# Performance work log

Measured on AMD Instinct MI355X. Metric: run time of the kernel, lower is better.

Reference implementation:

```python
import jax, jax.numpy as jnp
import numpy as np

B, U, V = 2, 32, 2048
IN_DIM, STATE, CODE = 256, 512, 256
H, HD = 8, 64
INNER = H * HD  # 512
HID = STATE     # ffn capacity_factor = 1.0


def layernorm(x, g, b, eps=1e-5):
    mu = jnp.mean(x, axis=-1, keepdims=True)
    var = jnp.var(x, axis=-1, keepdims=True)
    return (x - mu) * jax.lax.rsqrt(var + eps) * g + b


def setup_inputs() -> dict:
    key = jax.random.key(0)
    ks = jax.random.split(key, 24)
    s = 0.02
    inp = {
        'receiver_states': jax.random.normal(ks[0], (B, U, STATE), jnp.float32),
        'receiver_signatures': jax.random.normal(ks[1], (B, U, 64), jnp.float32),
        'receiver_codes': jax.random.normal(ks[2], (B, U, CODE), jnp.float32),
        'sender_states': jax.random.normal(ks[3], (B, V, IN_DIM), jnp.float32),
        # layernorms
        'ln_s_g': jnp.ones((IN_DIM,), jnp.float32), 'ln_s_b': jnp.zeros((IN_DIM,), jnp.float32),
        'ln_r_g': jnp.ones((STATE,), jnp.float32), 'ln_r_b': jnp.zeros((STATE,), jnp.float32),
        # ModFC query: in=STATE out=INNER ctx=CODE
        'Wq': jax.random.normal(ks[4], (INNER, STATE), jnp.float32) * s,
        'bq': jnp.zeros((INNER,), jnp.float32),
        'Cq': jax.random.normal(ks[5], (STATE, CODE), jnp.float32) * s,
        # ModFC key/value: in=IN_DIM out=INNER ctx=CODE
        'Wk': jax.random.normal(ks[6], (INNER, IN_DIM), jnp.float32) * s,
        'bk': jnp.zeros((INNER,), jnp.float32),
        'Ck': jax.random.normal(ks[7], (IN_DIM, CODE), jnp.float32) * s,
        'Wv': jax.random.normal(ks[8], (INNER, IN_DIM), jnp.float32) * s,
        'bv': jnp.zeros((INNER,), jnp.float32),
        'Cv': jax.random.normal(ks[9], (IN_DIM, CODE), jnp.float32) * s,
        # exit ModFC: in=INNER out=STATE ctx=CODE
        'We': jax.random.normal(ks[10], (STATE, INNER), jnp.float32) * s,
        'be': jnp.zeros((STATE,), jnp.float32),
        'Ce': jax.random.normal(ks[11], (INNER, CODE), jnp.float32) * s,
        'ls_attn': jnp.ones((STATE,), jnp.float32) * 1.0,
        # FFN
        'ln_f_g': jnp.ones((STATE,), jnp.float32), 'ln_f_b': jnp.zeros((STATE,), jnp.float32),
        'W1': jax.random.normal(ks[12], (HID, STATE), jnp.float32) * s,
        'b1': jnp.zeros((HID,), jnp.float32),
        'C1': jax.random.normal(ks[13], (STATE, CODE), jnp.float32) * s,
        'W2': jax.random.normal(ks[14], (STATE, HID), jnp.float32) * s,
        'b2': jnp.zeros((STATE,), jnp.float32),
        'C2': jax.random.normal(ks[15], (HID, CODE), jnp.float32) * s,
        'ls_ffn': jnp.ones((STATE,), jnp.float32) * 1e-6,
    }
    return inp


def reference(receiver_states, receiver_signatures, receiver_codes, sender_states,
              ln_s_g, ln_s_b, ln_r_g, ln_r_b,
              Wq, bq, Cq, Wk, bk, Ck, Wv, bv, Cv, We, be, Ce, ls_attn,
              ln_f_g, ln_f_b, W1, b1, C1, W2, b2, C2, ls_ffn):
    codes = receiver_codes  # (b,u,code)
    # --- ReadInAttention ---
    r_ln = layernorm(receiver_states, ln_r_g, ln_r_b)           # (b,u,state)
    s_ln = layernorm(sender_states, ln_s_g, ln_s_b)             # (b,v,in)
    # ModFC: y = linear(x * (1 + code @ C))
    # queries: (b,u,inner)
    q = jnp.einsum('bus,is->bui', r_ln * (1.0 + jnp.einsum('buc,sc->bus', codes, Cq)), Wq) + bq
    # per-receiver modulated senders: scale (b,u,in) broadcast over v
    scale_k = 1.0 + jnp.einsum('buc,ic->bui', codes, Ck)        # (b,u,in)
    scale_v = 1.0 + jnp.einsum('buc,ic->bui', codes, Cv)        # (b,u,in)
    mod_k = s_ln[:, :, None, :] * scale_k[:, None, :, :]        # (b,v,u,in)
    mod_v = s_ln[:, :, None, :] * scale_v[:, None, :, :]        # (b,v,u,in)
    keys = jnp.einsum('bvui,oi->bvuo', mod_k, Wk) + bk          # (b,v,u,inner)
    values = jnp.einsum('bvui,oi->bvuo', mod_v, Wv) + bv        # (b,v,u,inner)
    keys = keys.reshape(B, V, U, H, HD).transpose(0, 3, 2, 1, 4)    # (b,h,u,v,c)
    values = values.reshape(B, V, U, H, HD).transpose(0, 3, 2, 1, 4)
    qh = q.reshape(B, U, H, HD).transpose(0, 2, 1, 3)           # (b,h,u,c)
    scores = jnp.einsum('bhuc,bhuvc->bhuv', qh, keys) / np.sqrt(HD)
    attn = jax.nn.softmax(scores, axis=-1)
    msg = jnp.einsum('bhuv,bhuvc->bhuc', attn, values)          # (b,h,u,c)
    msg = msg.transpose(0, 2, 1, 3).reshape(B, U, INNER)        # (b,u,inner)
    msg = jnp.einsum('bui,oi->buo', msg * (1.0 + jnp.einsum('buc,ic->bui', codes, Ce)), We) + be
    attn_out = msg * ls_attn  # include_residual=False in read-in attention
    # --- ModFFN (residual) ---
    x = attn_out
    r = layernorm(x, ln_f_g, ln_f_b)
    h1 = jnp.einsum('bus,os->buo', r * (1.0 + jnp.einsum('buc,sc->bus', codes, C1)), W1) + b1
    h1 = jax.nn.gelu(h1, approximate=False)
    h2 = jnp.einsum('buh,oh->buo', h1 * (1.0 + jnp.einsum('buc,hc->buh', codes, C2)), W2) + b2
    out = x + h2 * ls_ffn
    return out
```

## Files before the change

### kernel.cpp

```cpp
#include <hip/hip_runtime.h>
#include <math.h>

#define B_ 2
#define U_ 32
#define V_ 2048
#define IN_ 256
#define ST_ 512
#define H_ 8
#define BU_ 64
#define NR_ 512

#define WS_SLN   0u
#define WS_SLNT  1048576u
#define WS_SCALE 2097152u
#define WS_T     2260992u
#define WS_CB    2392064u
#define WS_SSUMP 2392576u
#define WS_CTXP  2396672u
#define WS_AO    3445248u
#define WS_H2    3478016u
#define WS_AOP   3510784u

__device__ __forceinline__ float wsum(float v){
  #pragma unroll
  for(int m=32;m>0;m>>=1) v += __shfl_xor(v, m, 64);
  return v;
}

#define FMA4(A, t, S) { A.x += (t)*(S).x; A.y += (t)*(S).y; A.z += (t)*(S).z; A.w += (t)*(S).w; }

__global__ __launch_bounds__(256) void k_pre(const float* __restrict__ snd,
    const float* __restrict__ g, const float* __restrict__ bb,
    const float* __restrict__ codes,
    const float* __restrict__ Cq, const float* __restrict__ Ck, const float* __restrict__ Cv,
    const float* __restrict__ Ce, const float* __restrict__ C1, const float* __restrict__ C2,
    float* __restrict__ ws){
  __shared__ float tile[32][261];
  __shared__ float cds[8][256];
  const int tid = threadIdx.x;
  if(blockIdx.x < 128){
    const int wave = tid>>6, lane = tid&63;
    const int rowbase = blockIdx.x * 32;
    const int b = rowbase >> 11, vloc = rowbase & 2047;
    float4 gg  = *(const float4*)(g  + lane*4);
    float4 bbv = *(const float4*)(bb + lane*4);
    for(int it=0; it<8; ++it){
      int rl = it*4 + wave;
      int r  = rowbase + rl;
      float4 x = *(const float4*)(snd + (size_t)r*IN_ + lane*4);
      float s = x.x+x.y+x.z+x.w;
      float q = x.x*x.x+x.y*x.y+x.z*x.z+x.w*x.w;
      s = wsum(s); q = wsum(q);
      float mu = s*(1.0f/256.0f);
      float rv = rsqrtf(q*(1.0f/256.0f) - mu*mu + 1e-5f);
      float4 y;
      y.x = (x.x-mu)*rv*gg.x + bbv.x;
      y.y = (x.y-mu)*rv*gg.y + bbv.y;
      y.z = (x.z-mu)*rv*gg.z + bbv.z;
      y.w = (x.w-mu)*rv*gg.w + bbv.w;
      *(float4*)(ws + WS_SLN + (size_t)r*IN_ + lane*4) = y;
      tile[rl][lane*4+0] = y.x;
      tile[rl][lane*4+1] = y.y;
      tile[rl][lane*4+2] = y.z;
      tile[rl][lane*4+3] = y.w;
    }
    __syncthreads();
    const int vh = tid & 31;
    const int ibase = (tid >> 5);
    for(int it=0; it<32; ++it){
      int i = it*8 + ibase;
      ws[WS_SLNT + ((size_t)b*IN_ + i)*V_ + vloc + vh] = tile[vh][i];
    }
  } else {
    const int idx = blockIdx.x - 128;
    const int cg = idx % 40, bg = idx / 40;
    #pragma unroll
    for(int j=0;j<8;++j){
      int fi = j*256 + tid;
      cds[fi>>8][fi&255] = codes[(size_t)(bg*8)*256 + fi];
    }
    __syncthreads();
    const int q = tid & 3;
    const int col = cg*64 + (tid >> 2);
    const float* Cp; int loc;
    if(col < 512){ Cp = Cq; loc = col; }
    else if(col < 768){ Cp = Ck; loc = col - 512; }
    else if(col < 1024){ Cp = Cv; loc = col - 768; }
    else if(col < 1536){ Cp = Ce; loc = col - 1024; }
    else if(col < 2048){ Cp = C1; loc = col - 1536; }
    else { Cp = C2; loc = col - 2048; }
    const float4* wrow = (const float4*)(Cp + (size_t)loc*256 + q*64);
    float acc[8] = {0,0,0,0,0,0,0,0};
    #pragma unroll 4
    for(int i=0;i<16;++i){
      float4 w = wrow[i];
      #pragma unroll
      for(int k=0;k<8;++k){
        const float4 c = *(const float4*)(&cds[k][q*64 + i*4]);
        acc[k] += w.x*c.x + w.y*c.y + w.z*c.z + w.w*c.w;
      }
    }
    #pragma unroll
    for(int k=0;k<8;++k){
      acc[k] += __shfl_xor(acc[k], 1, 64);
      acc[k] += __shfl_xor(acc[k], 2, 64);
    }
    ws[WS_SCALE + (size_t)(bg*8 + q)*2560 + col]     = 1.0f + acc[q];
    ws[WS_SCALE + (size_t)(bg*8 + q + 4)*2560 + col] = 1.0f + acc[q+4];
  }
}

__global__ __launch_bounds__(256) void k_qt(const float* __restrict__ rst,
    const float* __restrict__ lg, const float* __restrict__ lb,
    const float* __restrict__ Wq, const float* __restrict__ bq,
    const float* __restrict__ Wk, const float* __restrict__ bk,
    float* __restrict__ ws){
  const int bu = blockIdx.x >> 3, h = blockIdx.x & 7;
  const int b = bu >> 5, u = bu & 31;
  const int r = (b*8 + h)*32 + u;
  const int tid = threadIdx.x, wave = tid>>6, lane = tid&63;
  __shared__ float xm[512];
  __shared__ float qv[64];
  __shared__ float red[4][65];
  __shared__ float rsm[4], rqm[4];
  float2 x2 = *(const float2*)(rst + (size_t)bu*512 + tid*2);
  float s = x2.x + x2.y, q = x2.x*x2.x + x2.y*x2.y;
  s = wsum(s); q = wsum(q);
  if(lane==0){ rsm[wave] = s; rqm[wave] = q; }
  __syncthreads();
  float S = rsm[0]+rsm[1]+rsm[2]+rsm[3];
  float Q = rqm[0]+rqm[1]+rqm[2]+rqm[3];
  float mu = S*(1.0f/512.0f);
  float rv = rsqrtf(Q*(1.0f/512.0f) - mu*mu + 1e-5f);
  const float* scal = ws + WS_SCALE + (size_t)bu*2560;
  xm[tid*2]   = ((x2.x-mu)*rv*lg[tid*2]   + lb[tid*2])   * scal[tid*2];
  xm[tid*2+1] = ((x2.y-mu)*rv*lg[tid*2+1] + lb[tid*2+1]) * scal[tid*2+1];
  __syncthreads();
  {
    const int o = tid & 63, sp = tid >> 6;
    const float4* wq = (const float4*)(Wq + (size_t)(h*64 + o)*512 + sp*128);
    const float* xp = xm + sp*128;
    float acc = 0.f;
    #pragma unroll 8
    for(int c4=0;c4<32;++c4){
      float4 w = wq[c4];
      acc += w.x*xp[c4*4] + w.y*xp[c4*4+1] + w.z*xp[c4*4+2] + w.w*xp[c4*4+3];
    }
    red[sp][o] = acc;
  }
  __syncthreads();
  if(tid < 64)
    qv[tid] = red[0][tid]+red[1][tid]+red[2][tid]+red[3][tid] + bq[h*64+tid];
  __syncthreads();
  if(tid < 64){
    float p = qv[tid] * bk[h*64+tid];
    p = wsum(p);
    if(tid==0) ws[WS_CB + r] = p;
  }
  {
    float acc = 0.f;
    #pragma unroll 4
    for(int d=0; d<64; ++d)
      acc += qv[d] * Wk[(size_t)(h*64+d)*256 + tid];
    ws[WS_T + (size_t)r*256 + tid] = acc * scal[512 + tid];
  }
}

__global__ __launch_bounds__(512) void k_scctx(const float* __restrict__ Tm, float* __restrict__ ws){
  const int rg = blockIdx.x >> 3, vc = blockIdx.x & 7;
  const int r0 = rg * 16;
  const int b  = rg >> 4;
  const int v0 = vc * 256;
  const int tid = threadIdx.x, lane = tid & 63;
  const int w  = __builtin_amdgcn_readfirstlane(tid >> 6);
  const int wr = w & 1, wk = w >> 1;
  const int rw8 = wr * 8;
  const int i0 = lane * 4;
  const int srow = tid >> 6;
  const int sf   = (tid & 63) * 4;

  __shared__ float P[16][256];
  __shared__ float stg[32][256];

  float4 a0={0,0,0,0},a1={0,0,0,0},a2={0,0,0,0},a3={0,0,0,0};
  float4 a4={0,0,0,0},a5={0,0,0,0},a6={0,0,0,0},a7={0,0,0,0};

  const float* Trow = Tm + (size_t)(r0 + rw8)*256;

  const float* p1base = ws + WS_SLNT + (size_t)b*IN_*V_ + v0;
  float4 g0,g1,g2,g3;
  g0 = *(const float4*)(p1base + (size_t)(srow    )*V_ + sf);
  g1 = *(const float4*)(p1base + (size_t)(srow+ 8)*V_ + sf);
  g2 = *(const float4*)(p1base + (size_t)(srow+16)*V_ + sf);
  g3 = *(const float4*)(p1base + (size_t)(srow+24)*V_ + sf);
  for(int s=0; s<8; ++s){
    __syncthreads();
    *(float4*)&stg[srow   ][sf] = g0;
    *(float4*)&stg[srow+ 8][sf] = g1;
    *(float4*)&stg[srow+16][sf] = g2;
    *(float4*)&stg[srow+24][sf] = g3;
    if(s < 7){
      const float* nb = p1base + (size_t)(s+1)*32*V_;
      g0 = *(const float4*)(nb + (size_t)(srow    )*V_ + sf);
      g1 = *(const float4*)(nb + (size_t)(srow+ 8)*V_ + sf);
      g2 = *(const float4*)(nb + (size_t)(srow+16)*V_ + sf);
      g3 = *(const float4*)(nb + (size_t)(srow+24)*V_ + sf);
    }
    const int kgA = s*32 + wk*8;
    float4 tA[8], tB[8];
    #pragma unroll
    for(int j=0;j<8;++j) tA[j] = *(const float4*)(Trow + (size_t)j*256 + kgA);
    __syncthreads();
    #pragma unroll
    for(int j=0;j<8;++j) tB[j] = *(const float4*)(Trow + (size_t)j*256 + kgA + 4);
    {
      const int kl = wk*8;
      float4 s0 = *(const float4*)&stg[kl+0][i0];
      float4 s1 = *(const float4*)&stg[kl+1][i0];
      float4 s2 = *(const float4*)&stg[kl+2][i0];
      float4 s3 = *(const float4*)&stg[kl+3][i0];
      FMA4(a0,tA[0].x,s0) FMA4(a0,tA[0].y,s1) FMA4(a0,tA[0].z,s2) FMA4(a0,tA[0].w,s3)
      FMA4(a1,tA[1].x,s0) FMA4(a1,tA[1].y,s1) FMA4(a1,tA[1].z,s2) FMA4(a1,tA[1].w,s3)
      FMA4(a2,tA[2].x,s0) FMA4(a2,tA[2].y,s1) FMA4(a2,tA[2].z,s2) FMA4(a2,tA[2].w,s3)
      FMA4(a3,tA[3].x,s0) FMA4(a3,tA[3].y,s1) FMA4(a3,tA[3].z,s2) FMA4(a3,tA[3].w,s3)
      FMA4(a4,tA[4].x,s0) FMA4(a4,tA[4].y,s1) FMA4(a4,tA[4].z,s2) FMA4(a4,tA[4].w,s3)
      FMA4(a5,tA[5].x,s0) FMA4(a5,tA[5].y,s1) FMA4(a5,tA[5].z,s2) FMA4(a5,tA[5].w,s3)
      FMA4(a6,tA[6].x,s0) FMA4(a6,tA[6].y,s1) FMA4(a6,tA[6].z,s2) FMA4(a6,tA[6].w,s3)
      FMA4(a7,tA[7].x,s0) FMA4(a7,tA[7].y,s1) FMA4(a7,tA[7].z,s2) FMA4(a7,tA[7].w,s3)
    }
    {
      const int kl = wk*8 + 4;
      float4 s0 = *(const float4*)&stg[kl+0][i0];
      float4 s1 = *(const float4*)&stg[kl+1][i0];
      float4 s2 = *(const float4*)&stg[kl+2][i0];
      float4 s3 = *(const float4*)&stg[kl+3][i0];
      FMA4(a0,tB[0].x,s0) FMA4(a0,tB[0].y,s1) FMA4(a0,tB[0].z,s2) FMA4(a0,tB[0].w,s3)
      FMA4(a1,tB[1].x,s0) FMA4(a1,tB[1].y,s1) FMA4(a1,tB[1].z,s2) FMA4(a1,tB[1].w,s3)
      FMA4(a2,tB[2].x,s0) FMA4(a2,tB[2].y,s1) FMA4(a2,tB[2].z,s2) FMA4(a2,tB[2].w,s3)
      FMA4(a3,tB[3].x,s0) FMA4(a3,tB[3].y,s1) FMA4(a3,tB[3].z,s2) FMA4(a3,tB[3].w,s3)
      FMA4(a4,tB[4].x,s0) FMA4(a4,tB[4].y,s1) FMA4(a4,tB[4].z,s2) FMA4(a4,tB[4].w,s3)
      FMA4(a5,tB[5].x,s0) FMA4(a5,tB[5].y,s1) FMA4(a5,tB[5].z,s2) FMA4(a5,tB[5].w,s3)
      FMA4(a6,tB[6].x,s0) FMA4(a6,tB[6].y,s1) FMA4(a6,tB[6].z,s2) FMA4(a6,tB[6].w,s3)
      FMA4(a7,tB[7].x,s0) FMA4(a7,tB[7].y,s1) FMA4(a7,tB[7].z,s2) FMA4(a7,tB[7].w,s3)
    }
  }
  __syncthreads();
  if(wk == 0){
    *(float4*)&P[rw8+0][i0]=a0; *(float4*)&P[rw8+1][i0]=a1;
    *(float4*)&P[rw8+2][i0]=a2; *(float4*)&P[rw8+3][i0]=a3;
    *(float4*)&P[rw8+4][i0]=a4; *(float4*)&P[rw8+5][i0]=a5;
    *(float4*)&P[rw8+6][i0]=a6; *(float4*)&P[rw8+7][i0]=a7;
  } else if(wk == 1){
    *(float4*)&stg[rw8+0][i0]=a0; *(float4*)&stg[rw8+1][i0]=a1;
    *(float4*)&stg[rw8+2][i0]=a2; *(float4*)&stg[rw8+3][i0]=a3;
    *(float4*)&stg[rw8+4][i0]=a4; *(float4*)&stg[rw8+5][i0]=a5;
    *(float4*)&stg[rw8+6][i0]=a6; *(float4*)&stg[rw8+7][i0]=a7;
  } else if(wk == 2){
    *(float4*)&stg[16+rw8+0][i0]=a0; *(float4*)&stg[16+rw8+1][i0]=a1;
    *(float4*)&stg[16+rw8+2][i0]=a2; *(float4*)&stg[16+rw8+3][i0]=a3;
    *(float4*)&stg[16+rw8+4][i0]=a4; *(float4*)&stg[16+rw8+5][i0]=a5;
    *(float4*)&stg[16+rw8+6][i0]=a6; *(float4*)&stg[16+rw8+7][i0]=a7;
  }
  __syncthreads();
  if(wk == 3){
    float4 av[8] = {a0,a1,a2,a3,a4,a5,a6,a7};
    #pragma unroll
    for(int j=0;j<8;++j){
      const int r = r0 + rw8 + j;
      const float cb = ws[WS_CB + r];
      float4 q0 = *(const float4*)&P[rw8+j][i0];
      float4 q1 = *(const float4*)&stg[rw8+j][i0];
      float4 q2 = *(const float4*)&stg[16+rw8+j][i0];
      float4 e;
      e.x = __expf((av[j].x+q0.x+q1.x+q2.x+cb)*0.125f);
      e.y = __expf((av[j].y+q0.y+q1.y+q2.y+cb)*0.125f);
      e.z = __expf((av[j].z+q0.z+q1.z+q2.z+cb)*0.125f);
      e.w = __expf((av[j].w+q0.w+q1.w+q2.w+cb)*0.125f);
      *(float4*)&P[rw8+j][i0] = e;
      float ss = wsum(e.x+e.y+e.z+e.w);
      if(lane==0) ws[WS_SSUMP + (size_t)r*8 + vc] = ss;
    }
  }

  a0=make_float4(0,0,0,0); a1=a0; a2=a0; a3=a0; a4=a0; a5=a0; a6=a0; a7=a0;
  const float* p2base = ws + WS_SLN + ((size_t)b*V_ + v0)*IN_;
  g0 = *(const float4*)(p2base + (size_t)(srow    )*IN_ + sf);
  g1 = *(const float4*)(p2base + (size_t)(srow+ 8)*IN_ + sf);
  g2 = *(const float4*)(p2base + (size_t)(srow+16)*IN_ + sf);
  g3 = *(const float4*)(p2base + (size_t)(srow+24)*IN_ + sf);
  for(int sv=0; sv<8; ++sv){
    __syncthreads();
    *(float4*)&stg[srow   ][sf] = g0;
    *(float4*)&stg[srow+ 8][sf] = g1;
    *(float4*)&stg[srow+16][sf] = g2;
    *(float4*)&stg[srow+24][sf] = g3;
    if(sv < 7){
      const float* nb = p2base + (size_t)(sv+1)*32*IN_;
      g0 = *(const float4*)(nb + (size_t)(srow    )*IN_ + sf);
      g1 = *(const float4*)(nb + (size_t)(srow+ 8)*IN_ + sf);
      g2 = *(const float4*)(nb + (size_t)(srow+16)*IN_ + sf);
      g3 = *(const float4*)(nb + (size_t)(srow+24)*IN_ + sf);
    }
    __syncthreads();
    {
      const int vl = wk*8, vg = sv*32 + vl;
      float4 p0_ = *(const float4*)&P[rw8+0][vg];
      float4 p1_ = *(const float4*)&P[rw8+1][vg];
      float4 p2_ = *(const float4*)&P[rw8+2][vg];
      float4 p3_ = *(const float4*)&P[rw8+3][vg];
      float4 p4_ = *(const float4*)&P[rw8+4][vg];
      float4 p5_ = *(const float4*)&P[rw8+5][vg];
      float4 p6_ = *(const float4*)&P[rw8+6][vg];
      float4 p7_ = *(const float4*)&P[rw8+7][vg];
      float4 s0 = *(const float4*)&stg[vl+0][i0];
      float4 s1 = *(const float4*)&stg[vl+1][i0];
      float4 s2 = *(const float4*)&stg[vl+2][i0];
      float4 s3 = *(const float4*)&stg[vl+3][i0];
      FMA4(a0,p0_.x,s0) FMA4(a0,p0_.y,s1) FMA4(a0,p0_.z,s2) FMA4(a0,p0_.w,s3)
      FMA4(a1,p1_.x,s0) FMA4(a1,p1_.y,s1) FMA4(a1,p1_.z,s2) FMA4(a1,p1_.w,s3)
      FMA4(a2,p2_.x,s0) FMA4(a2,p2_.y,s1) FMA4(a2,p2_.z,s2) FMA4(a2,p2_.w,s3)
      FMA4(a3,p3_.x,s0) FMA4(a3,p3_.y,s1) FMA4(a3,p3_.z,s2) FMA4(a3,p3_.w,s3)
      FMA4(a4,p4_.x,s0) FMA4(a4,p4_.y,s1) FMA4(a4,p4_.z,s2) FMA4(a4,p4_.w,s3)
      FMA4(a5,p5_.x,s0) FMA4(a5,p5_.y,s1) FMA4(a5,p5_.z,s2) FMA4(a5,p5_.w,s3)
      FMA4(a6,p6_.x,s0) FMA4(a6,p6_.y,s1) FMA4(a6,p6_.z,s2) FMA4(a6,p6_.w,s3)
      FMA4(a7,p7_.x,s0) FMA4(a7,p7_.y,s1) FMA4(a7,p7_.z,s2) FMA4(a7,p7_.w,s3)
    }
    {
      const int vl = wk*8 + 4, vg = sv*32 + vl;
      float4 p0_ = *(const float4*)&P[rw8+0][vg];
      float4 p1_ = *(const float4*)&P[rw8+1][vg];
      float4 p2_ = *(const float4*)&P[rw8+2][vg];
      float4 p3_ = *(const float4*)&P[rw8+3][vg];
      float4 p4_ = *(const float4*)&P[rw8+4][vg];
      float4 p5_ = *(const float4*)&P[rw8+5][vg];
      float4 p6_ = *(const float4*)&P[rw8+6][vg];
      float4 p7_ = *(const float4*)&P[rw8+7][vg];
      float4 s0 = *(const float4*)&stg[vl+0][i0];
      float4 s1 = *(const float4*)&stg[vl+1][i0];
      float4 s2 = *(const float4*)&stg[vl+2][i0];
      float4 s3 = *(const float4*)&stg[vl+3][i0];
      FMA4(a0,p0_.x,s0) FMA4(a0,p0_.y,s1) FMA4(a0,p0_.z,s2) FMA4(a0,p0_.w,s3)
      FMA4(a1,p1_.x,s0) FMA4(a1,p1_.y,s1) FMA4(a1,p1_.z,s2) FMA4(a1,p1_.w,s3)
      FMA4(a2,p2_.x,s0) FMA4(a2,p2_.y,s1) FMA4(a2,p2_.z,s2) FMA4(a2,p2_.w,s3)
      FMA4(a3,p3_.x,s0) FMA4(a3,p3_.y,s1) FMA4(a3,p3_.z,s2) FMA4(a3,p3_.w,s3)
      FMA4(a4,p4_.x,s0) FMA4(a4,p4_.y,s1) FMA4(a4,p4_.z,s2) FMA4(a4,p4_.w,s3)
      FMA4(a5,p5_.x,s0) FMA4(a5,p5_.y,s1) FMA4(a5,p5_.z,s2) FMA4(a5,p5_.w,s3)
      FMA4(a6,p6_.x,s0) FMA4(a6,p6_.y,s1) FMA4(a6,p6_.z,s2) FMA4(a6,p6_.w,s3)
      FMA4(a7,p7_.x,s0) FMA4(a7,p7_.y,s1) FMA4(a7,p7_.z,s2) FMA4(a7,p7_.w,s3)
    }
  }
  __syncthreads();
  if(wk == 0){
    *(float4*)&P[rw8+0][i0]=a0; *(float4*)&P[rw8+1][i0]=a1;
    *(float4*)&P[rw8+2][i0]=a2; *(float4*)&P[rw8+3][i0]=a3;
    *(float4*)&P[rw8+4][i0]=a4; *(float4*)&P[rw8+5][i0]=a5;
    *(float4*)&P[rw8+6][i0]=a6; *(float4*)&P[rw8+7][i0]=a7;
  } else if(wk == 1){
    *(float4*)&stg[rw8+0][i0]=a0; *(float4*)&stg[rw8+1][i0]=a1;
    *(float4*)&stg[rw8+2][i0]=a2; *(float4*)&stg[rw8+3][i0]=a3;
    *(float4*)&stg[rw8+4][i0]=a4; *(float4*)&stg[rw8+5][i0]=a5;
    *(float4*)&stg[rw8+6][i0]=a6; *(float4*)&stg[rw8+7][i0]=a7;
  } else if(wk == 2){
    *(float4*)&stg[16+rw8+0][i0]=a0; *(float4*)&stg[16+rw8+1][i0]=a1;
    *(float4*)&stg[16+rw8+2][i0]=a2; *(float4*)&stg[16+rw8+3][i0]=a3;
    *(float4*)&stg[16+rw8+4][i0]=a4; *(float4*)&stg[16+rw8+5][i0]=a5;
    *(float4*)&stg[16+rw8+6][i0]=a6; *(float4*)&stg[16+rw8+7][i0]=a7;
  }
  __syncthreads();
  if(wk == 3){
    float4 av[8] = {a0,a1,a2,a3,a4,a5,a6,a7};
    #pragma unroll
    for(int j=0;j<8;++j){
      const int r = r0 + rw8 + j;
      float4 q0 = *(const float4*)&P[rw8+j][i0];
      float4 q1 = *(const float4*)&stg[rw8+j][i0];
      float4 q2 = *(const float4*)&stg[16+rw8+j][i0];
      float4 d;
      d.x = av[j].x+q0.x+q1.x+q2.x;
      d.y = av[j].y+q0.y+q1.y+q2.y;
      d.z = av[j].z+q0.z+q1.z+q2.z;
      d.w = av[j].w+q0.w+q1.w+q2.w;
      *(float4*)(ws + WS_CTXP + ((size_t)vc*NR_ + r)*IN_ + i0) = d;
    }
  }
}

__global__ __launch_bounds__(512) void k_mexit(const float* __restrict__ Wv, const float* __restrict__ bv,
    const float* __restrict__ We, float* __restrict__ ws){
  const int bu = blockIdx.x >> 2, st = blockIdx.x & 3;
  const int b = bu >> 5, u = bu & 31;
  const int tid = threadIdx.x;
  __shared__ float xs[2][256];
  __shared__ float m2s[128];
  __shared__ float ps[4][128];
  __shared__ float invS[2];
  if(tid < 2){
    const int r = (b*8 + st*2 + tid)*32 + u;
    float v = 0.f;
    #pragma unroll
    for(int k=0;k<8;++k) v += ws[WS_SSUMP + (size_t)r*8 + k];
    invS[tid] = 1.0f / v;
  }
  {
    const int hh = tid >> 8, i = tid & 255;
    const int r = (b*8 + st*2 + hh)*32 + u;
    float s = 0.f;
    #pragma unroll
    for(int vcx=0; vcx<8; ++vcx)
      s += ws[WS_CTXP + ((size_t)vcx*NR_ + r)*IN_ + i];
    xs[hh][i] = s * ws[WS_SCALE + (size_t)bu*2560 + 768 + i];
  }
// ... 56 lines not shown
  __syncthreads();
  float S=rsm[0]+rsm[1]+rsm[2]+rsm[3], Q=rqm[0]+rqm[1]+rqm[2]+rqm[3];
  float mu = S*(1.0f/512.0f);
  float rv = rsqrtf(Q*(1.0f/512.0f) - mu*mu + 1e-5f);
  const float* scal = ws + WS_SCALE + (size_t)bu*2560;
  xr[s2]   = ((x2.x-mu)*rv*lg[s2]   + lb[s2])   * scal[1536 + s2];
  xr[s2+1] = ((x2.y-mu)*rv*lg[s2+1] + lb[s2+1]) * scal[1536 + s2+1];
  __syncthreads();
  const int o = ot*128 + (tid & 127), sp = tid >> 7;
  const float4* w1 = (const float4*)(W1 + (size_t)o*512 + sp*256);
  const float* xp = xr + sp*256;
  float acc = 0.f;
  #pragma unroll 8
  for(int c4=0;c4<64;++c4){
    float4 w = w1[c4];
    acc += w.x*xp[c4*4]+w.y*xp[c4*4+1]+w.z*xp[c4*4+2]+w.w*xp[c4*4+3];
  }
  ps[sp][tid&127] = acc;
  __syncthreads();
  if(sp==0){
    float hh = ps[0][tid] + ps[1][tid] + b1[o];
    float ge = 0.5f*hh*(1.0f + erff(hh*0.70710678118654752f));
    ws[WS_H2 + (size_t)bu*512 + o] = ge * scal[2048 + o];
  }
}

__global__ __launch_bounds__(256) void k_ffn2(const float* __restrict__ W2, const float* __restrict__ b2,
    const float* __restrict__ lsf, const float* __restrict__ ws, float* __restrict__ out){
  const int bu = blockIdx.x >> 2, st = blockIdx.x & 3;
  const int tid = threadIdx.x;
  const int s = st*128 + (tid & 127), sp = tid >> 7;
  __shared__ float ps[2][128];
  const float4* w2 = (const float4*)(W2 + (size_t)s*512 + sp*256);
  const float* hp = ws + WS_H2 + (size_t)bu*512 + sp*256;
  float acc = 0.f;
  #pragma unroll 8
  for(int c4=0;c4<64;++c4){
    float4 w = w2[c4];
    acc += w.x*hp[c4*4]+w.y*hp[c4*4+1]+w.z*hp[c4*4+2]+w.w*hp[c4*4+3];
  }
  ps[sp][tid&127] = acc;
  __syncthreads();
  if(sp==0)
    out[(size_t)bu*512 + s] = ws[WS_AO + (size_t)bu*512 + s]
                            + (ps[0][tid]+ps[1][tid] + b2[s]) * lsf[s];
}

extern "C" void kernel_launch(void* const* d_in, const int* in_sizes, int n_in,
                              void* d_out, int out_size, void* d_ws, size_t ws_size,
                              hipStream_t stream) {
  (void)in_sizes; (void)n_in; (void)out_size; (void)ws_size;
  const float* rst   = (const float*)d_in[0];
  const float* codes = (const float*)d_in[2];
  const float* snd   = (const float*)d_in[3];
  const float* ln_s_g = (const float*)d_in[4];
  const float* ln_s_b = (const float*)d_in[5];
  const float* ln_r_g = (const float*)d_in[6];
  const float* ln_r_b = (const float*)d_in[7];
  const float* Wq = (const float*)d_in[8];
  const float* bq = (const float*)d_in[9];
  const float* Cq = (const float*)d_in[10];
  const float* Wk = (const float*)d_in[11];
  const float* bk = (const float*)d_in[12];
  const float* Ck = (const float*)d_in[13];
  const float* Wv = (const float*)d_in[14];
  const float* bv = (const float*)d_in[15];
  const float* Cv = (const float*)d_in[16];
  const float* We = (const float*)d_in[17];
  const float* be = (const float*)d_in[18];
  const float* Ce = (const float*)d_in[19];
  const float* lsa = (const float*)d_in[20];
  const float* ln_f_g = (const float*)d_in[21];
  const float* ln_f_b = (const float*)d_in[22];
  const float* W1 = (const float*)d_in[23];
  const float* b1 = (const float*)d_in[24];
  const float* C1 = (const float*)d_in[25];
  const float* W2 = (const float*)d_in[26];
  const float* b2 = (const float*)d_in[27];
  const float* C2 = (const float*)d_in[28];
  const float* lsf = (const float*)d_in[29];
  float* ws  = (float*)d_ws;
  float* out = (float*)d_out;

  k_pre   <<<448, 256, 0, stream>>>(snd, ln_s_g, ln_s_b, codes, Cq, Ck, Cv, Ce, C1, C2, ws);
  k_qt    <<<512, 256, 0, stream>>>(rst, ln_r_g, ln_r_b, Wq, bq, Wk, bk, ws);
  k_scctx <<<256, 512, 0, stream>>>((const float*)(ws + WS_T), ws);
  k_mexit <<<256, 512, 0, stream>>>(Wv, bv, We, ws);
  k_ffn1  <<<256, 256, 0, stream>>>(be, lsa, ln_f_g, ln_f_b, W1, b1, ws);
  k_ffn2  <<<256, 256, 0, stream>>>(W2, b2, lsf, ws, out);
}
```

Measured before the change: 97.60 us.

## Fuse six kernel launches into one cooperative persistent kernel with grid syncs

Replaces the chain of six kernel launches with a single cooperative kernel of 256 blocks x 512 threads that runs each stage in turn, separated by grid.sync(). The aim is to remove per-launch overhead and the gaps between dependent kernels. The price is that stages with more parallelism (k_pre 448 blocks, k_qt 512 blocks) now squeeze into 256 blocks with reworked mappings, and grid-wide barriers carry their own cost. The old multi-kernel path is kept as a fallback if the cooperative launch fails.

```diff
diff --git a/kernel.cpp b/kernel.cpp
--- a/kernel.cpp
+++ b/kernel.cpp
@@ -1,5 +1,8 @@
 #include <hip/hip_runtime.h>
+#include <hip/hip_cooperative_groups.h>
 #include <math.h>
+
+namespace cg = cooperative_groups;
 
 #define B_ 2
 #define U_ 32
@@ -28,6 +31,486 @@
 }
 
 #define FMA4(A, t, S) { A.x += (t)*(S).x; A.y += (t)*(S).y; A.z += (t)*(S).z; A.w += (t)*(S).w; }
+
+struct P1S { float xm[2][512]; float qv[2][64]; float red[2][4][65]; float rsm[2][4]; float rqm[2][4]; };
+struct P2S { float P[16][256]; float stg[32][256]; };
+struct P3S { float xs[2][256]; float m2s[128]; float ps[4][128]; float invS[2]; };
+struct P4S { float xr[512]; float rsm[8]; float rqm[8]; float ps[4][128]; };
+union SMem {
+  float tile[32][257];
+  float cds[8][256];
+  P1S p1;
+  P2S p2;
+  P3S p3;
+  P4S p4;
+  float ps5[4][128];
+};
+
+__global__ __launch_bounds__(512) void k_all(
+    const float* __restrict__ rst, const float* __restrict__ codes, const float* __restrict__ snd,
+    const float* __restrict__ ln_s_g, const float* __restrict__ ln_s_b,
+    const float* __restrict__ ln_r_g, const float* __restrict__ ln_r_b,
+    const float* __restrict__ Wq, const float* __restrict__ bq, const float* __restrict__ Cq,
+    const float* __restrict__ Wk, const float* __restrict__ bk, const float* __restrict__ Ck,
+    const float* __restrict__ Wv, const float* __restrict__ bv, const float* __restrict__ Cv,
+    const float* __restrict__ We, const float* __restrict__ be, const float* __restrict__ Ce,
+    const float* __restrict__ lsa,
+    const float* __restrict__ ln_f_g, const float* __restrict__ ln_f_b,
+    const float* __restrict__ W1, const float* __restrict__ b1, const float* __restrict__ C1,
+    const float* __restrict__ W2, const float* __restrict__ b2, const float* __restrict__ C2,
+    const float* __restrict__ lsf,
+    float* __restrict__ ws, float* __restrict__ out){
+  cg::grid_group grid = cg::this_grid();
+  __shared__ SMem sm;
+  const int bid = blockIdx.x;
+  const int tid = threadIdx.x;
+  const int lane = tid & 63;
+
+  if(bid < 128){
+    const int wave = tid >> 6;
+    const int rowbase = bid * 32;
+    const int b = rowbase >> 11, vloc = rowbase & 2047;
+    float4 gg  = *(const float4*)(ln_s_g + lane*4);
+    float4 bbv = *(const float4*)(ln_s_b + lane*4);
+    #pragma unroll
+    for(int it=0; it<4; ++it){
+      int rl = it*8 + wave;
+      int r  = rowbase + rl;
+      float4 x = *(const float4*)(snd + (size_t)r*IN_ + lane*4);
+      float s = x.x+x.y+x.z+x.w;
+      float q = x.x*x.x+x.y*x.y+x.z*x.z+x.w*x.w;
+      s = wsum(s); q = wsum(q);
+      float mu = s*(1.0f/256.0f);
+      float rv = rsqrtf(q*(1.0f/256.0f) - mu*mu + 1e-5f);
+      float4 y;
+      y.x = (x.x-mu)*rv*gg.x + bbv.x;
+      y.y = (x.y-mu)*rv*gg.y + bbv.y;
+      y.z = (x.z-mu)*rv*gg.z + bbv.z;
+      y.w = (x.w-mu)*rv*gg.w + bbv.w;
+      *(float4*)(ws + WS_SLN + (size_t)r*IN_ + lane*4) = y;
+      sm.tile[rl][lane*4+0] = y.x;
+      sm.tile[rl][lane*4+1] = y.y;
+      sm.tile[rl][lane*4+2] = y.z;
+      sm.tile[rl][lane*4+3] = y.w;
+    }
+    __syncthreads();
+    const int vh = tid & 31, ig = tid >> 5;
+    #pragma unroll
+    for(int it=0; it<16; ++it){
+      int i = it*16 + ig;
+      ws[WS_SLNT + ((size_t)b*IN_ + i)*V_ + vloc + vh] = sm.tile[vh][i];
+    }
+  } else {
+    const int idx = bid - 128;
+    const int bg = idx >> 4, cg2 = idx & 15;
+    #pragma unroll
+    for(int j=0;j<4;++j){
+      int fi = j*512 + tid;
+      sm.cds[fi>>8][fi&255] = codes[(size_t)(bg*8)*256 + fi];
+    }
+    __syncthreads();
+    const int wave = tid >> 6;
+    const int q = lane & 3, cidx = lane >> 2;
+    #pragma unroll
+    for(int p=0; p<2; ++p){
+      const int coll = p*128 + wave*16 + cidx;
+      if(coll < 160){
+        const int col = cg2*160 + coll;
+        const float* Cp; int loc;
+        if(col < 512){ Cp = Cq; loc = col; }
+        else if(col < 768){ Cp = Ck; loc = col - 512; }
+        else if(col < 1024){ Cp = Cv; loc = col - 768; }
+        else if(col < 1536){ Cp = Ce; loc = col - 1024; }
+        else if(col < 2048){ Cp = C1; loc = col - 1536; }
+        else { Cp = C2; loc = col - 2048; }
+        const float4* wrow = (const float4*)(Cp + (size_t)loc*256 + q*64);
+        float acc[8] = {0,0,0,0,0,0,0,0};
+        #pragma unroll 4
+        for(int i=0;i<16;++i){
+          float4 w = wrow[i];
+          #pragma unroll
+          for(int k=0;k<8;++k){
+            const float4 c = *(const float4*)(&sm.cds[k][q*64 + i*4]);
+            acc[k] += w.x*c.x + w.y*c.y + w.z*c.z + w.w*c.w;
+          }
+        }
+        #pragma unroll
+        for(int k=0;k<8;++k){
+          acc[k] += __shfl_xor(acc[k], 1, 64);
+          acc[k] += __shfl_xor(acc[k], 2, 64);
+        }
+        ws[WS_SCALE + (size_t)(bg*8 + q)*2560 + col]     = 1.0f + acc[q];
+        ws[WS_SCALE + (size_t)(bg*8 + q + 4)*2560 + col] = 1.0f + acc[q+4];
+      }
+    }
+  }
+  grid.sync();
+
+  {
+    const int hb = tid >> 8, ltid = tid & 255;
+    const int vb = bid*2 + hb;
+    const int bu = vb >> 3, h = vb & 7;
+    const int b = bu >> 5, u = bu & 31;
+    const int r = (b*8 + h)*32 + u;
+    const int lw = ltid >> 6;
+    P1S& S1 = sm.p1;
+    float2 x2 = *(const float2*)(rst + (size_t)bu*512 + ltid*2);
+    float s = x2.x + x2.y, q = x2.x*x2.x + x2.y*x2.y;
+    s = wsum(s); q = wsum(q);
+    if(lane==0){ S1.rsm[hb][lw] = s; S1.rqm[hb][lw] = q; }
+    __syncthreads();
+    float S = S1.rsm[hb][0]+S1.rsm[hb][1]+S1.rsm[hb][2]+S1.rsm[hb][3];
+    float Q = S1.rqm[hb][0]+S1.rqm[hb][1]+S1.rqm[hb][2]+S1.rqm[hb][3];
+    float mu = S*(1.0f/512.0f);
+    float rv = rsqrtf(Q*(1.0f/512.0f) - mu*mu + 1e-5f);
+    const float* scal = ws + WS_SCALE + (size_t)bu*2560;
+    S1.xm[hb][ltid*2]   = ((x2.x-mu)*rv*ln_r_g[ltid*2]   + ln_r_b[ltid*2])   * scal[ltid*2];
+    S1.xm[hb][ltid*2+1] = ((x2.y-mu)*rv*ln_r_g[ltid*2+1] + ln_r_b[ltid*2+1]) * scal[ltid*2+1];
+    __syncthreads();
+    {
+      const int o = ltid & 63, sp = ltid >> 6;
+      const float4* wq = (const float4*)(Wq + (size_t)(h*64 + o)*512 + sp*128);
+      const float* xp = &S1.xm[hb][sp*128];
+      float acc = 0.f;
+      #pragma unroll 8
+      for(int c4=0;c4<32;++c4){
+        float4 w = wq[c4];
+        acc += w.x*xp[c4*4] + w.y*xp[c4*4+1] + w.z*xp[c4*4+2] + w.w*xp[c4*4+3];
+      }
+      S1.red[hb][sp][o] = acc;
+    }
+    __syncthreads();
+    if(ltid < 64)
+      S1.qv[hb][ltid] = S1.red[hb][0][ltid]+S1.red[hb][1][ltid]+S1.red[hb][2][ltid]+S1.red[hb][3][ltid]
+                      + bq[h*64+ltid];
+    __syncthreads();
+    if(ltid < 64){
+      float p = S1.qv[hb][ltid] * bk[h*64+ltid];
+      p = wsum(p);
+      if(ltid==0) ws[WS_CB + r] = p;
+    }
+    {
+      float acc = 0.f;
+      #pragma unroll 4
+      for(int d=0; d<64; ++d)
+        acc += S1.qv[hb][d] * Wk[(size_t)(h*64+d)*256 + ltid];
+      ws[WS_T + (size_t)r*256 + ltid] = acc * scal[512 + ltid];
+    }
+  }
+  grid.sync();
+
+  {
+    const int rg = bid >> 3, vc = bid & 7;
+    const int r0 = rg * 16;
+    const int b  = rg >> 4;
+    const int v0 = vc * 256;
+    const int w  = __builtin_amdgcn_readfirstlane(tid >> 6);
+    const int wr = w & 1, wk = w >> 1;
+    const int rw8 = wr * 8;
+    const int i0 = lane * 4;
+    const int srow = tid >> 6;
+    const int sf   = (tid & 63) * 4;
+    float (*P)[256]   = sm.p2.P;
+    float (*stg)[256] = sm.p2.stg;
+    const float* Tm = ws + WS_T;
+
+    float4 a0={0,0,0,0},a1={0,0,0,0},a2={0,0,0,0},a3={0,0,0,0};
+    float4 a4={0,0,0,0},a5={0,0,0,0},a6={0,0,0,0},a7={0,0,0,0};
+    const float* Trow = Tm + (size_t)(r0 + rw8)*256;
+
+    const float* p1base = ws + WS_SLNT + (size_t)b*IN_*V_ + v0;
+    float4 g0,g1,g2,g3;
+    g0 = *(const float4*)(p1base + (size_t)(srow    )*V_ + sf);
+    g1 = *(const float4*)(p1base + (size_t)(srow+ 8)*V_ + sf);
+    g2 = *(const float4*)(p1base + (size_t)(srow+16)*V_ + sf);
+    g3 = *(const float4*)(p1base + (size_t)(srow+24)*V_ + sf);
+    for(int s=0; s<8; ++s){
+      __syncthreads();
+      *(float4*)&stg[srow   ][sf] = g0;
+      *(float4*)&stg[srow+ 8][sf] = g1;
+      *(float4*)&stg[srow+16][sf] = g2;
+      *(float4*)&stg[srow+24][sf] = g3;
+      if(s < 7){
+        const float* nb = p1base + (size_t)(s+1)*32*V_;
+        g0 = *(const float4*)(nb + (size_t)(srow    )*V_ + sf);
+        g1 = *(const float4*)(nb + (size_t)(srow+ 8)*V_ + sf);
+        g2 = *(const float4*)(nb + (size_t)(srow+16)*V_ + sf);
+        g3 = *(const float4*)(nb + (size_t)(srow+24)*V_ + sf);
+      }
+      const int kgA = s*32 + wk*8;
+      float4 tA[8], tB[8];
+      #pragma unroll
+      for(int j=0;j<8;++j) tA[j] = *(const float4*)(Trow + (size_t)j*256 + kgA);
+      __syncthreads();
+      #pragma unroll
+      for(int j=0;j<8;++j) tB[j] = *(const float4*)(Trow + (size_t)j*256 + kgA + 4);
+      {
+        const int kl = wk*8;
+        float4 s0 = *(const float4*)&stg[kl+0][i0];
+        float4 s1 = *(const float4*)&stg[kl+1][i0];
+        float4 s2 = *(const float4*)&stg[kl+2][i0];
+        float4 s3 = *(const float4*)&stg[kl+3][i0];
+        FMA4(a0,tA[0].x,s0) FMA4(a0,tA[0].y,s1) FMA4(a0,tA[0].z,s2) FMA4(a0,tA[0].w,s3)
+        FMA4(a1,tA[1].x,s0) FMA4(a1,tA[1].y,s1) FMA4(a1,tA[1].z,s2) FMA4(a1,tA[1].w,s3)
+        FMA4(a2,tA[2].x,s0) FMA4(a2,tA[2].y,s1) FMA4(a2,tA[2].z,s2) FMA4(a2,tA[2].w,s3)
+        FMA4(a3,tA[3].x,s0) FMA4(a3,tA[3].y,s1) FMA4(a3,tA[3].z,s2) FMA4(a3,tA[3].w,s3)
+        FMA4(a4,tA[4].x,s0) FMA4(a4,tA[4].y,s1) FMA4(a4,tA[4].z,s2) FMA4(a4,tA[4].w,s3)
+        FMA4(a5,tA[5].x,s0) FMA4(a5,tA[5].y,s1) FMA4(a5,tA[5].z,s2) FMA4(a5,tA[5].w,s3)
+        FMA4(a6,tA[6].x,s0) FMA4(a6,tA[6].y,s1) FMA4(a6,tA[6].z,s2) FMA4(a6,tA[6].w,s3)
+        FMA4(a7,tA[7].x,s0) FMA4(a7,tA[7].y,s1) FMA4(a7,tA[7].z,s2) FMA4(a7,tA[7].w,s3)
+      }
+      {
+        const int kl = wk*8 + 4;
+        float4 s0 = *(const float4*)&stg[kl+0][i0];
+        float4 s1 = *(const float4*)&stg[kl+1][i0];
+        float4 s2 = *(const float4*)&stg[kl+2][i0];
+        float4 s3 = *(const float4*)&stg[kl+3][i0];
+        FMA4(a0,tB[0].x,s0) FMA4(a0,tB[0].y,s1) FMA4(a0,tB[0].z,s2) FMA4(a0,tB[0].w,s3)
+        FMA4(a1,tB[1].x,s0) FMA4(a1,tB[1].y,s1) FMA4(a1,tB[1].z,s2) FMA4(a1,tB[1].w,s3)
+        FMA4(a2,tB[2].x,s0) FMA4(a2,tB[2].y,s1) FMA4(a2,tB[2].z,s2) FMA4(a2,tB[2].w,s3)
+        FMA4(a3,tB[3].x,s0) FMA4(a3,tB[3].y,s1) FMA4(a3,tB[3].z,s2) FMA4(a3,tB[3].w,s3)
+        FMA4(a4,tB[4].x,s0) FMA4(a4,tB[4].y,s1) FMA4(a4,tB[4].z,s2) FMA4(a4,tB[4].w,s3)
+        FMA4(a5,tB[5].x,s0) FMA4(a5,tB[5].y,s1) FMA4(a5,tB[5].z,s2) FMA4(a5,tB[5].w,s3)
+        FMA4(a6,tB[6].x,s0) FMA4(a6,tB[6].y,s1) FMA4(a6,tB[6].z,s2) FMA4(a6,tB[6].w,s3)
+        FMA4(a7,tB[7].x,s0) FMA4(a7,tB[7].y,s1) FMA4(a7,tB[7].z,s2) FMA4(a7,tB[7].w,s3)
+      }
+    }
+    __syncthreads();
+    if(wk == 0){
+      *(float4*)&P[rw8+0][i0]=a0; *(float4*)&P[rw8+1][i0]=a1;
+      *(float4*)&P[rw8+2][i0]=a2; *(float4*)&P[rw8+3][i0]=a3;
+      *(float4*)&P[rw8+4][i0]=a4; *(float4*)&P[rw8+5][i0]=a5;
+      *(float4*)&P[rw8+6][i0]=a6; *(float4*)&P[rw8+7][i0]=a7;
+    } else if(wk == 1){
+      *(float4*)&stg[rw8+0][i0]=a0; *(float4*)&stg[rw8+1][i0]=a1;
+      *(float4*)&stg[rw8+2][i0]=a2; *(float4*)&stg[rw8+3][i0]=a3;
+      *(float4*)&stg[rw8+4][i0]=a4; *(float4*)&stg[rw8+5][i0]=a5;
+      *(float4*)&stg[rw8+6][i0]=a6; *(float4*)&stg[rw8+7][i0]=a7;
+    } else if(wk == 2){
+      *(float4*)&stg[16+rw8+0][i0]=a0; *(float4*)&stg[16+rw8+1][i0]=a1;
+      *(float4*)&stg[16+rw8+2][i0]=a2; *(float4*)&stg[16+rw8+3][i0]=a3;
+      *(float4*)&stg[16+rw8+4][i0]=a4; *(float4*)&stg[16+rw8+5][i0]=a5;
+      *(float4*)&stg[16+rw8+6][i0]=a6; *(float4*)&stg[16+rw8+7][i0]=a7;
+    }
+    __syncthreads();
+    if(wk == 3){
+      float4 av[8] = {a0,a1,a2,a3,a4,a5,a6,a7};
+      #pragma unroll
+      for(int j=0;j<8;++j){
+        const int r = r0 + rw8 + j;
+        const float cb = ws[WS_CB + r];
+        float4 q0 = *(const float4*)&P[rw8+j][i0];
+        float4 q1 = *(const float4*)&stg[rw8+j][i0];
+        float4 q2 = *(const float4*)&stg[16+rw8+j][i0];
+        float4 e;
+        e.x = __expf((av[j].x+q0.x+q1.x+q2.x+cb)*0.125f);
+        e.y = __expf((av[j].y+q0.y+q1.y+q2.y+cb)*0.125f);
+        e.z = __expf((av[j].z+q0.z+q1.z+q2.z+cb)*0.125f);
+        e.w = __expf((av[j].w+q0.w+q1.w+q2.w+cb)*0.125f);
+        *(float4*)&P[rw8+j][i0] = e;
+        float ss = wsum(e.x+e.y+e.z+e.w);
+        if(lane==0) ws[WS_SSUMP + (size_t)r*8 + vc] = ss;
+      }
+    }
+
+    a0=make_float4(0,0,0,0); a1=a0; a2=a0; a3=a0; a4=a0; a5=a0; a6=a0; a7=a0;
+    const float* p2base = ws + WS_SLN + ((size_t)b*V_ + v0)*IN_;
+    g0 = *(const float4*)(p2base + (size_t)(srow    )*IN_ + sf);
+    g1 = *(const float4*)(p2base + (size_t)(srow+ 8)*IN_ + sf);
+    g2 = *(const float4*)(p2base + (size_t)(srow+16)*IN_ + sf);
+    g3 = *(const float4*)(p2base + (size_t)(srow+24)*IN_ + sf);
+    for(int sv=0; sv<8; ++sv){
+      __syncthreads();
+      *(float4*)&stg[srow   ][sf] = g0;
+      *(float4*)&stg[srow+ 8][sf] = g1;
+      *(float4*)&stg[srow+16][sf] = g2;
+      *(float4*)&stg[srow+24][sf] = g3;
+      if(sv < 7){
+        const float* nb = p2base + (size_t)(sv+1)*32*IN_;
+        g0 = *(const float4*)(nb + (size_t)(srow    )*IN_ + sf);
+        g1 = *(const float4*)(nb + (size_t)(srow+ 8)*IN_ + sf);
+        g2 = *(const float4*)(nb + (size_t)(srow+16)*IN_ + sf);
+        g3 = *(const float4*)(nb + (size_t)(srow+24)*IN_ + sf);
+      }
+      __syncthreads();
+      #pragma unroll
+      for(int half=0; half<2; ++half){
+        const int vl = wk*8 + half*4, vg = sv*32 + vl;
+        float4 p0_ = *(const float4*)&P[rw8+0][vg];
+        float4 p1_ = *(const float4*)&P[rw8+1][vg];
+        float4 p2_ = *(const float4*)&P[rw8+2][vg];
+        float4 p3_ = *(const float4*)&P[rw8+3][vg];
+        float4 p4_ = *(const float4*)&P[rw8+4][vg];
+        float4 p5_ = *(const float4*)&P[rw8+5][vg];
+        float4 p6_ = *(const float4*)&P[rw8+6][vg];
+        float4 p7_ = *(const float4*)&P[rw8+7][vg];
+        float4 s0 = *(const float4*)&stg[vl+0][i0];
+        float4 s1 = *(const float4*)&stg[vl+1][i0];
+        float4 s2 = *(const float4*)&stg[vl+2][i0];
+        float4 s3 = *(const float4*)&stg[vl+3][i0];
+        FMA4(a0,p0_.x,s0) FMA4(a0,p0_.y,s1) FMA4(a0,p0_.z,s2) FMA4(a0,p0_.w,s3)
+        FMA4(a1,p1_.x,s0) FMA4(a1,p1_.y,s1) FMA4(a1,p1_.z,s2) FMA4(a1,p1_.w,s3)
+        FMA4(a2,p2_.x,s0) FMA4(a2,p2_.y,s1) FMA4(a2,p2_.z,s2) FMA4(a2,p2_.w,s3)
+        FMA4(a3,p3_.x,s0) FMA4(a3,p3_.y,s1) FMA4(a3,p3_.z,s2) FMA4(a3,p3_.w,s3)
+        FMA4(a4,p4_.x,s0) FMA4(a4,p4_.y,s1) FMA4(a4,p4_.z,s2) FMA4(a4,p4_.w,s3)
+        FMA4(a5,p5_.x,s0) FMA4(a5,p5_.y,s1) FMA4(a5,p5_.z,s2) FMA4(a5,p5_.w,s3)
+        FMA4(a6,p6_.x,s0) FMA4(a6,p6_.y,s1) FMA4(a6,p6_.z,s2) FMA4(a6,p6_.w,s3)
+        FMA4(a7,p7_.x,s0) FMA4(a7,p7_.y,s1) FMA4(a7,p7_.z,s2) FMA4(a7,p7_.w,s3)
+      }
+    }
+    __syncthreads();
+    if(wk == 0){
+      *(float4*)&P[rw8+0][i0]=a0; *(float4*)&P[rw8+1][i0]=a1;
+      *(float4*)&P[rw8+2][i0]=a2; *(float4*)&P[rw8+3][i0]=a3;
+      *(float4*)&P[rw8+4][i0]=a4; *(float4*)&P[rw8+5][i0]=a5;
+      *(float4*)&P[rw8+6][i0]=a6; *(float4*)&P[rw8+7][i0]=a7;
+    } else if(wk == 1){
+      *(float4*)&stg[rw8+0][i0]=a0; *(float4*)&stg[rw8+1][i0]=a1;
+      *(float4*)&stg[rw8+2][i0]=a2; *(float4*)&stg[rw8+3][i0]=a3;
+      *(float4*)&stg[rw8+4][i0]=a4; *(float4*)&stg[rw8+5][i0]=a5;
+      *(float4*)&stg[rw8+6][i0]=a6; *(float4*)&stg[rw8+7][i0]=a7;
+    } else if(wk == 2){
+      *(float4*)&stg[16+rw8+0][i0]=a0; *(float4*)&stg[16+rw8+1][i0]=a1;
+      *(float4*)&stg[16+rw8+2][i0]=a2; *(float4*)&stg[16+rw8+3][i0]=a3;
+      *(float4*)&stg[16+rw8+4][i0]=a4; *(float4*)&stg[16+rw8+5][i0]=a5;
+      *(float4*)&stg[16+rw8+6][i0]=a6; *(float4*)&stg[16+rw8+7][i0]=a7;
+    }
+    __syncthreads();
+    if(wk == 3){
+      float4 av[8] = {a0,a1,a2,a3,a4,a5,a6,a7};
+      #pragma unroll
+      for(int j=0;j<8;++j){
+        const int r = r0 + rw8 + j;
+        float4 q0 = *(const float4*)&P[rw8+j][i0];
+        float4 q1 = *(const float4*)&stg[rw8+j][i0];
+        float4 q2 = *(const float4*)&stg[16+rw8+j][i0];
+        float4 d;
+        d.x = av[j].x+q0.x+q1.x+q2.x;
+        d.y = av[j].y+q0.y+q1.y+q2.y;
+        d.z = av[j].z+q0.z+q1.z+q2.z;
+        d.w = av[j].w+q0.w+q1.w+q2.w;
+        *(float4*)(ws + WS_CTXP + ((size_t)vc*NR_ + r)*IN_ + i0) = d;
+      }
+    }
+  }
+  grid.sync();
+
+  {
+    const int bu = bid >> 2, st = bid & 3;
+    const int b = bu >> 5, u = bu & 31;
+    P3S& S3 = sm.p3;
+    if(tid < 2){
+      const int r = (b*8 + st*2 + tid)*32 + u;
+      float v = 0.f;
+      #pragma unroll
+      for(int k=0;k<8;++k) v += ws[WS_SSUMP + (size_t)r*8 + k];
+      S3.invS[tid] = 1.0f / v;
+    }
+    {
+      const int hh = tid >> 8, i = tid & 255;
+      const int r = (b*8 + st*2 + hh)*32 + u;
+      float s = 0.f;
+      #pragma unroll
+      for(int vcx=0; vcx<8; ++vcx)
+        s += ws[WS_CTXP + ((size_t)vcx*NR_ + r)*IN_ + i];
+      S3.xs[hh][i] = s * ws[WS_SCALE + (size_t)bu*2560 + 768 + i];
+    }
+    __syncthreads();
+    {
+      const int lo = tid & 127, sp = tid >> 7;
+      const int o = st*128 + lo;
+      const float4* wv = (const float4*)(Wv + (size_t)o*256 + sp*64);
+      const float* xp = &S3.xs[lo>>6][sp*64];
+      float acc = 0.f;
+      #pragma unroll
+      for(int c4=0;c4<16;++c4){
+        float4 w = wv[c4];
+        acc += w.x*xp[c4*4]+w.y*xp[c4*4+1]+w.z*xp[c4*4+2]+w.w*xp[c4*4+3];
+      }
+      S3.ps[sp][lo] = acc;
+    }
+    __syncthreads();
+    if(tid < 128){
+      const int o = st*128 + tid;
+      S3.m2s[tid] = ((S3.ps[0][tid]+S3.ps[1][tid]+S3.ps[2][tid]+S3.ps[3][tid]) * S3.invS[tid>>6] + bv[o])
+                    * ws[WS_SCALE + (size_t)bu*2560 + 1024 + o];
+    }
+    __syncthreads();
+    {
+      const float4* we = (const float4*)(We + (size_t)tid*512 + st*128);
+      float acc = 0.f;
+      #pragma unroll 8
+      for(int c4=0;c4<32;++c4){
+        float4 w = we[c4];
+        acc += w.x*S3.m2s[c4*4]+w.y*S3.m2s[c4*4+1]+w.z*S3.m2s[c4*4+2]+w.w*S3.m2s[c4*4+3];
+      }
+      ws[WS_AOP + ((size_t)st*BU_ + bu)*512 + tid] = acc;
+    }
+  }
+  grid.sync();
+
+  {
+    const int bu = bid >> 2, ot = bid & 3;
+    P4S& S4 = sm.p4;
+    const float* scal = ws + WS_SCALE + (size_t)bu*2560;
+    const float* aop = ws + WS_AOP;
+    float ax = aop[((size_t)0*BU_+bu)*512 + tid]
+             + aop[((size_t)1*BU_+bu)*512 + tid]
+             + aop[((size_t)2*BU_+bu)*512 + tid]
+             + aop[((size_t)3*BU_+bu)*512 + tid];
+    float xv = (ax + be[tid]) * lsa[tid];
+    if(ot == 0) ws[WS_AO + (size_t)bu*512 + tid] = xv;
+    float s = wsum(xv), q = wsum(xv*xv);
+    if(lane==0){ S4.rsm[tid>>6] = s; S4.rqm[tid>>6] = q; }
+    __syncthreads();
+    float S = 0.f, Q = 0.f;
+    #pragma unroll
+    for(int k=0;k<8;++k){ S += S4.rsm[k]; Q += S4.rqm[k]; }
+    float mu = S*(1.0f/512.0f);
+    float rv = rsqrtf(Q*(1.0f/512.0f) - mu*mu + 1e-5f);
+    S4.xr[tid] = ((xv-mu)*rv*ln_f_g[tid] + ln_f_b[tid]) * scal[1536 + tid];
+    __syncthreads();
+    const int o = ot*128 + (tid & 127), sp = tid >> 7;
+    const float4* w1 = (const float4*)(W1 + (size_t)o*512 + sp*128);
+    const float* xp = S4.xr + sp*128;
+    float acc = 0.f;
+    #pragma unroll 8
+    for(int c4=0;c4<32;++c4){
+      float4 w = w1[c4];
+      acc += w.x*xp[c4*4]+w.y*xp[c4*4+1]+w.z*xp[c4*4+2]+w.w*xp[c4*4+3];
+    }
+    S4.ps[sp][tid&127] = acc;
+    __syncthreads();
+    if(tid < 128){
+      const int oo = ot*128 + tid;
+      float hh = S4.ps[0][tid]+S4.ps[1][tid]+S4.ps[2][tid]+S4.ps[3][tid] + b1[oo];
+      float ge = 0.5f*hh*(1.0f + erff(hh*0.70710678118654752f));
+      ws[WS_H2 + (size_t)bu*512 + oo] = ge * scal[2048 + oo];
+    }
+  }
+  grid.sync();
+
+  {
+    const int bu = bid >> 2, st = bid & 3;
+    const int lo = tid & 127, sp = tid >> 7;
+    const int s = st*128 + lo;
+    const float4* w2 = (const float4*)(W2 + (size_t)s*512 + sp*128);
+    const float* hp = ws + WS_H2 + (size_t)bu*512 + sp*128;
+    float acc = 0.f;
+    #pragma unroll 8
+    for(int c4=0;c4<32;++c4){
+      float4 w = w2[c4];
+      acc += w.x*hp[c4*4]+w.y*hp[c4*4+1]+w.z*hp[c4*4+2]+w.w*hp[c4*4+3];
+    }
+    sm.ps5[sp][lo] = acc;
+    __syncthreads();
+    if(tid < 128){
+      const int ss = st*128 + tid;
+      out[(size_t)bu*512 + ss] = ws[WS_AO + (size_t)bu*512 + ss]
+        + (sm.ps5[0][tid]+sm.ps5[1][tid]+sm.ps5[2][tid]+sm.ps5[3][tid] + b2[ss]) * lsf[ss];
+    }
+  }
+}
 
 __global__ __launch_bounds__(256) void k_pre(const float* __restrict__ snd,
     const float* __restrict__ g, const float* __restrict__ bb,
@@ -178,15 +661,11 @@
   const int i0 = lane * 4;
   const int srow = tid >> 6;
   const int sf   = (tid & 63) * 4;
-
   __shared__ float P[16][256];
   __shared__ float stg[32][256];
-
   float4 a0={0,0,0,0},a1={0,0,0,0},a2={0,0,0,0},a3={0,0,0,0};
   float4 a4={0,0,0,0},a5={0,0,0,0},a6={0,0,0,0},a7={0,0,0,0};
-
   const float* Trow = Tm + (size_t)(r0 + rw8)*256;
-
   const float* p1base = ws + WS_SLNT + (size_t)b*IN_*V_ + v0;
   float4 g0,g1,g2,g3;
   g0 = *(const float4*)(p1base + (size_t)(srow    )*V_ + sf);
@@ -281,7 +760,6 @@
       if(lane==0) ws[WS_SSUMP + (size_t)r*8 + vc] = ss;
     }
   }
-
   a0=make_float4(0,0,0,0); a1=a0; a2=a0; a3=a0; a4=a0; a5=a0; a6=a0; a7=a0;
   const float* p2base = ws + WS_SLN + ((size_t)b*V_ + v0)*IN_;
   g0 = *(const float4*)(p2base + (size_t)(srow    )*IN_ + sf);
@@ -302,31 +780,9 @@
       g3 = *(const float4*)(nb + (size_t)(srow+24)*IN_ + sf);
     }
     __syncthreads();
-    {
-      const int vl = wk*8, vg = sv*32 + vl;
-      float4 p0_ = *(const float4*)&P[rw8+0][vg];
-      float4 p1_ = *(const float4*)&P[rw8+1][vg];
-      float4 p2_ = *(const float4*)&P[rw8+2][vg];
-      float4 p3_ = *(const float4*)&P[rw8+3][vg];
-      float4 p4_ = *(const float4*)&P[rw8+4][vg];
-      float4 p5_ = *(const float4*)&P[rw8+5][vg];
-      float4 p6_ = *(const float4*)&P[rw8+6][vg];
-      float4 p7_ = *(const float4*)&P[rw8+7][vg];
-      float4 s0 = *(const float4*)&stg[vl+0][i0];
-      float4 s1 = *(const float4*)&stg[vl+1][i0];
-      float4 s2 = *(const float4*)&stg[vl+2][i0];
-      float4 s3 = *(const float4*)&stg[vl+3][i0];
-      FMA4(a0,p0_.x,s0) FMA4(a0,p0_.y,s1) FMA4(a0,p0_.z,s2) FMA4(a0,p0_.w,s3)
-      FMA4(a1,p1_.x,s0) FMA4(a1,p1_.y,s1) FMA4(a1,p1_.z,s2) FMA4(a1,p1_.w,s3)
-      FMA4(a2,p2_.x,s0) FMA4(a2,p2_.y,s1) FMA4(a2,p2_.z,s2) FMA4(a2,p2_.w,s3)
-      FMA4(a3,p3_.x,s0) FMA4(a3,p3_.y,s1) FMA4(a3,p3_.z,s2) FMA4(a3,p3_.w,s3)
-      FMA4(a4,p4_.x,s0) FMA4(a4,p4_.y,s1) FMA4(a4,p4_.z,s2) FMA4(a4,p4_.w,s3)
-      FMA4(a5,p5_.x,s0) FMA4(a5,p5_.y,s1) FMA4(a5,p5_.z,s2) FMA4(a5,p5_.w,s3)
-      FMA4(a6,p6_.x,s0) FMA4(a6,p6_.y,s1) FMA4(a6,p6_.z,s2) FMA4(a6,p6_.w,s3)
-      FMA4(a7,p7_.x,s0) FMA4(a7,p7_.y,s1) FMA4(a7,p7_.z,s2) FMA4(a7,p7_.w,s3)
-    }
-    {
-      const int vl = wk*8 + 4, vg = sv*32 + vl;
+    #pragma unroll
+    for(int half=0; half<2; ++half){
+      const int vl = wk*8 + half*4, vg = sv*32 + vl;
       float4 p0_ = *(const float4*)&P[rw8+0][vg];
       float4 p1_ = *(const float4*)&P[rw8+1][vg];
       float4 p2_ = *(const float4*)&P[rw8+2][vg];
@@ -549,10 +1005,29 @@
   float* ws  = (float*)d_ws;
   float* out = (float*)d_out;
 
-  k_pre   <<<448, 256, 0, stream>>>(snd, ln_s_g, ln_s_b, codes, Cq, Ck, Cv, Ce, C1, C2, ws);
-  k_qt    <<<512, 256, 0, stream>>>(rst, ln_r_g, ln_r_b, Wq, bq, Wk, bk, ws);
-  k_scctx <<<256, 512, 0, stream>>>((const float*)(ws + WS_T), ws);
-  k_mexit <<<256, 512, 0, stream>>>(Wv, bv, We, ws);
-  k_ffn1  <<<256, 256, 0, stream>>>(be, lsa, ln_f_g, ln_f_b, W1, b1, ws);
-  k_ffn2  <<<256, 256, 0, stream>>>(W2, b2, lsf, ws, out);
+  void* args[] = {
+    (void*)&rst, (void*)&codes, (void*)&snd,
+    (void*)&ln_s_g, (void*)&ln_s_b, (void*)&ln_r_g, (void*)&ln_r_b,
+    (void*)&Wq, (void*)&bq, (void*)&Cq,
+    (void*)&Wk, (void*)&bk, (void*)&Ck,
+    (void*)&Wv, (void*)&bv, (void*)&Cv,
+    (void*)&We, (void*)&be, (void*)&Ce,
+    (void*)&lsa,
+    (void*)&ln_f_g, (void*)&ln_f_b,
+    (void*)&W1, (void*)&b1, (void*)&C1,
+    (void*)&W2, (void*)&b2, (void*)&C2,
+    (void*)&lsf,
+    (void*)&ws, (void*)&out
+  };
+  hipError_t err = hipLaunchCooperativeKernel(reinterpret_cast<void*>(k_all),
+                                              dim3(256), dim3(512), args, 0, stream);
+  if(err != hipSuccess){
+    (void)hipGetLastError();
+    k_pre   <<<448, 256, 0, stream>>>(snd, ln_s_g, ln_s_b, codes, Cq, Ck, Cv, Ce, C1, C2, ws);
+    k_qt    <<<512, 256, 0, stream>>>(rst, ln_r_g, ln_r_b, Wq, bq, Wk, bk, ws);
+    k_scctx <<<256, 512, 0, stream>>>((const float*)(ws + WS_T), ws);
+    k_mexit <<<256, 512, 0, stream>>>(Wv, bv, We, ws);
+    k_ffn1  <<<256, 256, 0, stream>>>(be, lsa, ln_f_g, ln_f_b, W1, b1, ws);
+    k_ffn2  <<<256, 256, 0, stream>>>(W2, b2, lsf, ws, out);
+  }
 }
```

Measured after the change: 254.0 us. +160.3%, slower.
